# Kernel optimization log

Hardware: AMD Instinct MI355X
Metric: run time of the kernel (lower is better)

## Reference

```python
import jax, jax.numpy as jnp
import numpy as np

B, S, D, H = 4, 2048, 768, 8
HD = D // H
EPS = 1e-5
NEG = -1e9


def setup_inputs() -> dict:
    key = jax.random.key(0)
    ks = jax.random.split(key, 12)
    s = 1.0 / np.sqrt(D)
    inp = {
        "hidden_states": jax.random.normal(ks[0], (B, S, D), dtype=jnp.float32),
        "anchor_mask": jax.random.bernoulli(ks[1], 0.5, (B, S)),
        "ln_g": jnp.ones((D,), jnp.float32),
        "ln_b": jnp.zeros((D,), jnp.float32),
        "Wq": jax.random.uniform(ks[2], (D, D), jnp.float32, -s, s),
        "bq": jax.random.uniform(ks[3], (D,), jnp.float32, -s, s),
        "Wk": jax.random.uniform(ks[4], (D, D), jnp.float32, -s, s),
        "bk": jax.random.uniform(ks[5], (D,), jnp.float32, -s, s),
        "Wv": jax.random.uniform(ks[6], (D, D), jnp.float32, -s, s),
        "bv": jax.random.uniform(ks[7], (D,), jnp.float32, -s, s),
        "Wo": jax.random.uniform(ks[8], (D, D), jnp.float32, -s, s),
        "bo": jax.random.uniform(ks[9], (D,), jnp.float32, -s, s),
    }
    return inp


def reference(hidden_states, anchor_mask, ln_g, ln_b, Wq, bq, Wk, bk, Wv, bv, Wo, bo):
    # LayerNorm (per-token, so applying to all tokens == applying to gathered anchors)
    mu = jnp.mean(hidden_states, axis=-1, keepdims=True)
    var = jnp.mean(jnp.square(hidden_states - mu), axis=-1, keepdims=True)
    x = (hidden_states - mu) * jax.lax.rsqrt(var + EPS) * ln_g + ln_b

    # QKV projections: torch Linear is x @ W.T + b
    q = (jnp.einsum('bsd,ed->bse', x, Wq) + bq).reshape(B, S, H, HD)
    k = (jnp.einsum('bsd,ed->bse', x, Wk) + bk).reshape(B, S, H, HD)
    v = (jnp.einsum('bsd,ed->bse', x, Wv) + bv).reshape(B, S, H, HD)

    scale = 1.0 / np.sqrt(HD)
    scores = jnp.einsum('bqhd,bkhd->bhqk', q, k) * scale
    # keys restricted to anchor positions (equivalent to the gather)
    key_mask = anchor_mask[:, None, None, :]  # (B,1,1,S)
    scores = jnp.where(key_mask, scores, NEG)
    attn = jax.nn.softmax(scores, axis=-1)  # dropout is identity in eval

    out = jnp.einsum('bhqk,bkhd->bqhd', attn, v).reshape(B, S, D)
    out = jnp.einsum('bsd,ed->bse', out, Wo) + bo
    # scatter back: zeros at non-anchor positions
    return out * anchor_mask[:, :, None].astype(out.dtype)
```

## Files before the change

kernel.cpp:

```cpp
#include <hip/hip_runtime.h>
#include <math.h>

#define S_LEN 2048
#define D_DIM 768
#define NH 8
#define HD 96
#define NTOK 8192

typedef short bf16x8 __attribute__((ext_vector_type(8)));
typedef float f32x4 __attribute__((ext_vector_type(4)));
typedef float f32x16 __attribute__((ext_vector_type(16)));
typedef unsigned int u32x2 __attribute__((ext_vector_type(2)));
typedef unsigned int u32x4 __attribute__((ext_vector_type(4)));

__device__ __forceinline__ f32x4 mfma16(bf16x8 a, bf16x8 b, f32x4 c) {
    return __builtin_amdgcn_mfma_f32_16x16x32_bf16(a, b, c, 0, 0, 0);
}
__device__ __forceinline__ f32x16 mfma32(bf16x8 a, bf16x8 b, f32x16 c) {
    return __builtin_amdgcn_mfma_f32_32x32x16_bf16(a, b, c, 0, 0, 0);
}

__device__ __forceinline__ unsigned short f2bf(float f) {
    unsigned int u = __float_as_uint(f);
    u += 0x7fffu + ((u >> 16) & 1u);
    return (unsigned short)(u >> 16);
}

__device__ __forceinline__ unsigned int cvtpk(float lo, float hi) {
    unsigned int r;
    asm("v_cvt_pk_bf16_f32 %0, %1, %2" : "=v"(r) : "v"(lo), "v"(hi));
    return r;
}

__device__ __forceinline__ void gl_lds16(const unsigned short* g, unsigned short* l) {
    __builtin_amdgcn_global_load_lds(
        (const __attribute__((address_space(1))) unsigned int*)g,
        (__attribute__((address_space(3))) unsigned int*)l, 16, 0, 0);
}

#define TILE_SHORTS 6144
#define BH_SHORTS   196608

__global__ __launch_bounds__(256) void prep_kernel(
    const unsigned char* __restrict__ mb, int* __restrict__ idx, int* __restrict__ cnt,
    const float* __restrict__ Wq, const float* __restrict__ Wk,
    const float* __restrict__ Wv, const float* __restrict__ Wo,
    unsigned short* __restrict__ W4b, float* __restrict__ out)
{
    const int bi = blockIdx.x;
    const int t  = threadIdx.x;

    if (bi < 4) {
        __shared__ int red[4];
        __shared__ int warp_tot[4];
        const int b = bi;
        int s = 0;
        for (int i = t; i < NTOK; i += 256) s += (int)mb[i];
        for (int off = 32; off > 0; off >>= 1) s += __shfl_down(s, off, 64);
        if ((t & 63) == 0) red[t >> 6] = s;
        __syncthreads();
        const int total = red[0] + red[1] + red[2] + red[3];
        const int mode = (total > 20000) ? 2 : ((total > 2500) ? 1 : 0);
        const int*   mi = (const int*)mb;
        const float* mf = (const float*)mb;
        const int p0 = t * 8;
        int av = 0, c = 0;
        #pragma unroll
        for (int j = 0; j < 8; ++j) {
            const int g = b * S_LEN + p0 + j;
            bool a;
            if (mode == 2)      a = (mf[g] != 0.0f);
            else if (mode == 1) a = (mb[g] != 0);
            else                a = (mi[g] != 0);
            if (a) { av |= (1 << j); ++c; }
        }
        const int lane = t & 63, w = t >> 6;
        int v = c;
        #pragma unroll
        for (int off = 1; off < 64; off <<= 1) {
            const int u = __shfl_up(v, off, 64);
            if (lane >= off) v += u;
        }
        if (lane == 63) warp_tot[w] = v;
        __syncthreads();
        int wbase = 0;
        for (int i = 0; i < w; ++i) wbase += warp_tot[i];
        int o = wbase + v - c;
        #pragma unroll
        for (int j = 0; j < 8; ++j)
            if (av & (1 << j)) idx[b * S_LEN + (o++)] = p0 + j;
        if (t == 255) cnt[b] = wbase + v;
    } else if (bi < 1156) {
        const int i = bi - 4;
        const int w = i / 288, blk = i % 288;
        const float* src = (w == 0) ? Wq : (w == 1) ? Wk : (w == 2) ? Wv : Wo;
        const int base = (blk * 256 + t) * 8;
        const float4 a = *(const float4*)&src[base];
        const float4 c = *(const float4*)&src[base + 4];
        uint4 u;
        u.x = (unsigned int)f2bf(a.x) | ((unsigned int)f2bf(a.y) << 16);
        u.y = (unsigned int)f2bf(a.z) | ((unsigned int)f2bf(a.w) << 16);
        u.z = (unsigned int)f2bf(c.x) | ((unsigned int)f2bf(c.y) << 16);
        u.w = (unsigned int)f2bf(c.z) | ((unsigned int)f2bf(c.w) << 16);
        *(uint4*)&W4b[(size_t)w * 589824 + base] = u;
    } else {
        const size_t i4 = (size_t)(bi - 1156) * 256 + t;
        float4 z; z.x = z.y = z.z = z.w = 0.0f;
        *(float4*)&out[i4 * 4] = z;
    }
}

__global__ __launch_bounds__(256) void ln_gather_kernel(
    const float* __restrict__ H, const float* __restrict__ g,
    const float* __restrict__ bta, const int* __restrict__ idx,
    const int* __restrict__ cnt, unsigned short* __restrict__ X)
{
    __shared__ float rs[4], rss[4];
    const int slot = blockIdx.x;
    const int b = slot >> 11, r = slot & (S_LEN - 1);
    if (r >= cnt[b]) return;
    const int p = idx[slot];
    const float* hr = H + (size_t)(b * S_LEN + p) * D_DIM;
    unsigned short* xr = X + (size_t)slot * D_DIM;
    const int t = threadIdx.x;
    const float v0 = hr[t], v1 = hr[t + 256], v2 = hr[t + 512];
    float s  = v0 + v1 + v2;
    float ss = v0*v0 + v1*v1 + v2*v2;
    for (int off = 32; off > 0; off >>= 1) {
        s  += __shfl_down(s,  off, 64);
        ss += __shfl_down(ss, off, 64);
    }
    if ((t & 63) == 0) { rs[t >> 6] = s; rss[t >> 6] = ss; }
    __syncthreads();
    const float sum = rs[0] + rs[1] + rs[2] + rs[3];
    const float sq  = rss[0] + rss[1] + rss[2] + rss[3];
    const float mu  = sum * (1.0f / D_DIM);
    const float var = sq * (1.0f / D_DIM) - mu * mu;
    const float rstd = rsqrtf(var + 1e-5f);
    xr[t]       = f2bf((v0 - mu) * rstd * g[t]       + bta[t]);
    xr[t + 256] = f2bf((v1 - mu) * rstd * g[t + 256] + bta[t + 256]);
    xr[t + 512] = f2bf((v2 - mu) * rstd * g[t + 512] + bta[t + 512]);
}

__global__ __launch_bounds__(256) void gemm_bf16(
    const unsigned short* __restrict__ A,
    const unsigned short* __restrict__ W4,
    const float* __restrict__ b0, const float* __restrict__ b1,
    const float* __restrict__ b2,
    const int* __restrict__ cnt, const int* __restrict__ idx,
    unsigned short* __restrict__ Qo, unsigned short* __restrict__ Kp,
    unsigned short* __restrict__ Vp, float* __restrict__ Fo,
    int oproj)
{
    const int z = blockIdx.z;
    const int m0 = blockIdx.y * 64;
    const int b  = m0 >> 11;
    const int rbase = m0 & (S_LEN - 1);
    const int nc = cnt[b];
    if (rbase >= nc) return;
    const int n0 = blockIdx.x * 128;
    const unsigned short* W = W4 + (size_t)z * 589824;
    const float* bias = (z == 0) ? b0 : (z == 1 ? b1 : b2);

    __shared__ unsigned short Al[2][64 * 32];
    __shared__ unsigned short Bl[2][128 * 32];

    const int t = threadIdx.x;
    const int srow = t >> 2, sg = t & 3;
    const int ra0 = b * S_LEN + min(rbase + srow, nc - 1);
    const unsigned short* gA0 = A + (size_t)ra0 * 768 + sg * 8;
    const unsigned short* gB0 = W + (size_t)(n0 + srow)      * 768 + sg * 8;
    const unsigned short* gB1 = W + (size_t)(n0 + srow + 64) * 768 + sg * 8;
    const int t8 = t * 8;

    const int w = t >> 6, lane = t & 63;
    const int l15 = lane & 15, quad = lane >> 4;
    const int mh = (w & 1) * 32, nh2 = (w >> 1) * 64;

    f32x4 acc[2][4] = {};

    int aoff[2], boff[4];
    #pragma unroll
    for (int i = 0; i < 2; ++i) aoff[i] = (mh  + i * 16 + l15) * 32 + quad * 8;
    #pragma unroll
    for (int i = 0; i < 4; ++i) boff[i] = (nh2 + i * 16 + l15) * 32 + quad * 8;

    gl_lds16(gA0, &Al[0][t8]);
    gl_lds16(gB0, &Bl[0][t8]);
    gl_lds16(gB1, &Bl[0][2048 + t8]);
    __syncthreads();

    for (int it = 0; it < 24; ++it) {
        const int cur = it & 1;
        if (it + 1 < 24) {
            const int k1 = (it + 1) * 32;
            gl_lds16(gA0 + k1, &Al[cur ^ 1][t8]);
            gl_lds16(gB0 + k1, &Bl[cur ^ 1][t8]);
            gl_lds16(gB1 + k1, &Bl[cur ^ 1][2048 + t8]);
        }
        bf16x8 af[2], bfr[4];
        #pragma unroll
        for (int i = 0; i < 2; ++i) af[i]  = *(const bf16x8*)(&Al[cur][aoff[i]]);
        #pragma unroll
        for (int i = 0; i < 4; ++i) bfr[i] = *(const bf16x8*)(&Bl[cur][boff[i]]);
        #pragma unroll
        for (int ms = 0; ms < 2; ++ms)
            #pragma unroll
            for (int ns = 0; ns < 4; ++ns)
                acc[ms][ns] = mfma16(af[ms], bfr[ns], acc[ms][ns]);
        __syncthreads();
    }

    if (!oproj) {
        if (z == 0) {
            #pragma unroll
            for (int ns = 0; ns < 4; ++ns) {
                const int n = n0 + nh2 + ns * 16 + l15;
                const float bv = bias[n];
                #pragma unroll
                for (int ms = 0; ms < 2; ++ms) {
                    const int ml = mh + ms * 16 + quad * 4;
                    #pragma unroll
                    for (int r = 0; r < 4; ++r) {
                        const int slot = b * S_LEN + rbase + ml + r;
                        Qo[(size_t)slot * 768 + n] = f2bf(acc[ms][ns][r] + bv);
                    }
                }
            }
        } else if (z == 1) {
            #pragma unroll
            for (int ns = 0; ns < 4; ++ns) {
                const int n = n0 + nh2 + ns * 16 + l15;
                const int h = n / 96, d = n - h * 96;
                const float bv = bias[n];
                unsigned short* base = Kp + (size_t)(b * 8 + h) * BH_SHORTS;
                const int dseg = d >> 3, dlo = d & 7;
                #pragma unroll
                for (int ms = 0; ms < 2; ++ms) {
                    const int ml = mh + ms * 16 + quad * 4;
                    #pragma unroll
                    for (int r = 0; r < 4; ++r) {
                        const int tok = rbase + ml + r;
                        const int kt = tok >> 6, tk = tok & 63;
                        const int g16 = tk >> 4, lr = tk & 15;
                        base[(size_t)kt * TILE_SHORTS +
                             (g16 * 192 + dseg * 16 + lr) * 8 + dlo] =
                            (tok < nc) ? f2bf(acc[ms][ns][r] + bv)
                                       : (unsigned short)0;
                    }
                }
            }
        } else {
            #pragma unroll
            for (int ns = 0; ns < 4; ++ns) {
                const int n = n0 + nh2 + ns * 16 + l15;
                const int h = n / 96, d = n - h * 96;
                const float bv = bias[n];
                unsigned short* base = Vp + (size_t)(b * 8 + h) * BH_SHORTS;
                const int dg = d >> 4, l16 = d & 15;
                #pragma unroll
                for (int ms = 0; ms < 2; ++ms) {
                    const int ml = mh + ms * 16 + quad * 4;
                    const int k = rbase + ml;
                    const int kt = k >> 6, tk = k & 63;
                    const int kseg = tk >> 3, klo = tk & 7;
                    const unsigned short h0 =
                        (k + 0 < nc) ? f2bf(acc[ms][ns][0] + bv) : (unsigned short)0;
                    const unsigned short h1 =
                        (k + 1 < nc) ? f2bf(acc[ms][ns][1] + bv) : (unsigned short)0;
                    const unsigned short h2 =
                        (k + 2 < nc) ? f2bf(acc[ms][ns][2] + bv) : (unsigned short)0;
                    const unsigned short h3 =
                        (k + 3 < nc) ? f2bf(acc[ms][ns][3] + bv) : (unsigned short)0;
                    uint2 u;
                    u.x = (unsigned int)h0 | ((unsigned int)h1 << 16);
                    u.y = (unsigned int)h2 | ((unsigned int)h3 << 16);
                    *(uint2*)&base[(size_t)kt * TILE_SHORTS +
                                   (dg * 128 + kseg * 16 + l16) * 8 + klo] = u;
                }
            }
        }
    } else {
        #pragma unroll
        for (int ns = 0; ns < 4; ++ns) {
            const int n = n0 + nh2 + ns * 16 + l15;
            const float bv = bias[n];
            #pragma unroll
            for (int ms = 0; ms < 2; ++ms) {
                const int ml = mh + ms * 16 + quad * 4;
                #pragma unroll
                for (int r = 0; r < 4; ++r) {
                    const int rloc = rbase + ml + r;
                    if (rloc < nc) {
                        const int orow = b * S_LEN + idx[b * S_LEN + rloc];
                        Fo[(size_t)orow * 768 + n] = acc[ms][ns][r] + bv;
                    }
                }
            }
        }
    }
}

__global__ __launch_bounds__(256) void attn_mfma(
    const unsigned short* __restrict__ Q,
    const unsigned short* __restrict__ Kp,
    const unsigned short* __restrict__ Vp,
    const int* __restrict__ cnt,
    unsigned short* __restrict__ O)
{
    const int bh = blockIdx.x & 31;
    const int b  = bh >> 3, h = bh & 7;
    const int q0 = (blockIdx.x >> 5) * 32;
    const int nk = cnt[b];
    if (q0 >= nk) return;

    __shared__ f32x4 CMB4[2][64][13];

    const int t = threadIdx.x, w = t >> 6, lane = t & 63;
    const int l15 = lane & 15;
    const int gh  = (lane >> 4) & 1;
    const int hi  = lane >> 5;
    const int q32 = lane & 31;
    const int bS  = b * S_LEN;
    const float CE = 0.14724459f;

    const unsigned short* Kg = Kp + (size_t)(b * 8 + h) * BH_SHORTS;
    const unsigned short* Vg = Vp + (size_t)(b * 8 + h) * BH_SHORTS;

    const unsigned short* qrow = Q + (size_t)(bS + q0 + q32) * 768 + h * 96 + hi * 8;
    bf16x8 qf[6];
    #pragma unroll
    for (int ks = 0; ks < 6; ++ks) qf[ks] = *(const bf16x8*)(qrow + ks * 16);

    const int kb0 = (gh * 192 + hi * 16 + l15) * 8;
    const int vb0 = (gh * 128 + hi * 16 + l15) * 8;

    float ls0 = 0.0f, ls1 = 0.0f;
    f32x16 oacc[3] = {};

    const int kts = (nk + 63) >> 6;

    if (w < kts) {
        const unsigned short* Kt0 = Kg + (size_t)w * TILE_SHORTS + kb0;
        bf16x8 kfc[6];
        #pragma unroll
        for (int ks = 0; ks < 6; ++ks)
            kfc[ks] = *(const bf16x8*)(Kt0 + (ks * 32) * 8);

        for (int kt = w; kt < kts; kt += 4) {
            const unsigned short* Kt = Kg + (size_t)kt * TILE_SHORTS + kb0;
            const unsigned short* Vt = Vg + (size_t)kt * TILE_SHORTS + vb0;

            #pragma unroll
            for (int s = 0; s < 2; ++s) {
                const unsigned short* Kn = (s == 0)
                    ? (Kt + 384 * 8)
                    : (Kt + (size_t)4 * TILE_SHORTS);
                bf16x8 kfn[6];
                #pragma unroll
                for (int ks = 0; ks < 6; ++ks)
                    kfn[ks] = *(const bf16x8*)(Kn + (ks * 32) * 8);

                f32x16 sa = {};
                __builtin_amdgcn_s_setprio(1);
                #pragma unroll
                for (int ks = 0; ks < 6; ++ks) sa = mfma32(kfc[ks], qf[ks], sa);
                __builtin_amdgcn_s_setprio(0);

                unsigned int wv[8];
                #pragma unroll
                for (int j = 0; j < 8; ++j) {
                    const float e0 = exp2f(sa[2 * j]     * CE);
                    const float e1 = exp2f(sa[2 * j + 1] * CE);
                    if (j & 1) ls1 += e0 + e1; else ls0 += e0 + e1;
                    wv[j] = cvtpk(e0, e1);
                }
                const u32x2 r02 = __builtin_amdgcn_permlane32_swap(wv[0], wv[2], false, false);
                const u32x2 r13 = __builtin_amdgcn_permlane32_swap(wv[1], wv[3], false, false);
                const u32x2 r46 = __builtin_amdgcn_permlane32_swap(wv[4], wv[6], false, false);
                const u32x2 r57 = __builtin_amdgcn_permlane32_swap(wv[5], wv[7], false, false);
                const u32x4 pw0 = { r02.x, r13.x, r02.y, r13.y };
                const u32x4 pw1 = { r46.x, r57.x, r46.y, r57.y };
                const bf16x8 pb0 = __builtin_bit_cast(bf16x8, pw0);
                const bf16x8 pb1 = __builtin_bit_cast(bf16x8, pw1);

                const int kkb = s * 2;
                __builtin_amdgcn_s_setprio(1);
                #pragma unroll
                for (int dg = 0; dg < 3; ++dg) {
                    const bf16x8 v0 = *(const bf16x8*)(Vt + (dg * 256 + kkb * 32) * 8);
                    const bf16x8 v1 = *(const bf16x8*)(Vt + (dg * 256 + (kkb + 1) * 32) * 8);
                    oacc[dg] = mfma32(v0, pb0, oacc[dg]);
                    oacc[dg] = mfma32(v1, pb1, oacc[dg]);
                }
                __builtin_amdgcn_s_setprio(0);

                #pragma unroll
                for (int ks = 0; ks < 6; ++ks) kfc[ks] = kfn[ks];
            }
        }
    }

    float lsum = ls0 + ls1;
    lsum += __shfl_xor(lsum, 32);

    if (w >= 2) {
        f32x4* dst = CMB4[w - 2][lane];
        #pragma unroll
        for (int dg = 0; dg < 3; ++dg)
            #pragma unroll
            for (int m = 0; m < 4; ++m) {
                const f32x4 p = { oacc[dg][4 * m],     oacc[dg][4 * m + 1],
                                  oacc[dg][4 * m + 2], oacc[dg][4 * m + 3] };
                dst[dg * 4 + m] = p;
            }
        const f32x4 tl = { lsum, 0.0f, 0.0f, 0.0f };
        dst[12] = tl;
    }
    __syncthreads();
    if (w < 2) {
        const f32x4* src = CMB4[w][lane];
        #pragma unroll
        for (int dg = 0; dg < 3; ++dg)
            #pragma unroll
            for (int m = 0; m < 4; ++m) {
                const f32x4 p = src[dg * 4 + m];
                #pragma unroll
                for (int j = 0; j < 4; ++j) oacc[dg][4 * m + j] += p[j];
            }
        lsum += src[12][0];
    }
    __syncthreads();
    if (w == 1) {
        f32x4* dst = CMB4[0][lane];
        #pragma unroll
        for (int dg = 0; dg < 3; ++dg)
            #pragma unroll
            for (int m = 0; m < 4; ++m) {
                const f32x4 p = { oacc[dg][4 * m],     oacc[dg][4 * m + 1],
                                  oacc[dg][4 * m + 2], oacc[dg][4 * m + 3] };
                dst[dg * 4 + m] = p;
            }
        const f32x4 tl = { lsum, 0.0f, 0.0f, 0.0f };
        dst[12] = tl;
    }
    __syncthreads();
    if (w > 0) return;

    {
        const f32x4* src = CMB4[0][lane];
        #pragma unroll
        for (int dg = 0; dg < 3; ++dg)
            #pragma unroll
            for (int m = 0; m < 4; ++m) {
                const f32x4 p = src[dg * 4 + m];
                #pragma unroll
                for (int j = 0; j < 4; ++j) oacc[dg][4 * m + j] += p[j];
            }
        lsum += src[12][0];
    }
    lsum -= (float)((kts << 6) - nk);

    const int qi = q0 + q32;
    if (qi < nk) {
        const float rl = 1.0f / lsum;
        unsigned short* og = O + (size_t)(bS + qi) * 768 + h * 96;
        #pragma unroll
        for (int dg = 0; dg < 3; ++dg) {
            #pragma unroll
            for (int m = 0; m < 4; ++m) {
                uint2 u;
                u.x = cvtpk(oacc[dg][4 * m]     * rl, oacc[dg][4 * m + 1] * rl);
                u.y = cvtpk(oacc[dg][4 * m + 2] * rl, oacc[dg][4 * m + 3] * rl);
                *(uint2*)&og[dg * 32 + m * 8 + hi * 4] = u;
            }
        }
    }
}

extern "C" void kernel_launch(void* const* d_in, const int* in_sizes, int n_in,
                              void* d_out, int out_size, void* d_ws, size_t ws_size,
                              hipStream_t stream)
{
    const float* hs  = (const float*)d_in[0];
    const unsigned char* am = (const unsigned char*)d_in[1];
    const float* lng = (const float*)d_in[2];
    const float* lnb = (const float*)d_in[3];
    const float* Wq  = (const float*)d_in[4];
    const float* bq  = (const float*)d_in[5];
    const float* Wk  = (const float*)d_in[6];
    const float* bk  = (const float*)d_in[7];
    const float* Wv  = (const float*)d_in[8];
    const float* bv  = (const float*)d_in[9];
    const float* Wo  = (const float*)d_in[10];
    const float* bo  = (const float*)d_in[11];

    char* ws = (char*)d_ws;
    const size_t BUF = (size_t)NTOK * 768 * 2;
    int* idx = (int*)ws;
    int* cnt = (int*)(ws + 32768);
    unsigned short* xb  = (unsigned short*)(ws + 65536);
    unsigned short* Qb  = (unsigned short*)(ws + 65536 + BUF);
    unsigned short* Kpb = (unsigned short*)(ws + 65536 + 2 * BUF);
    unsigned short* Vpb = (unsigned short*)(ws + 65536 + 3 * BUF);
    unsigned short* W4b = (unsigned short*)(ws + 65536 + 4 * BUF);
    unsigned short* Ob  = xb;
    float* out = (float*)d_out;

    prep_kernel<<<dim3(2692), dim3(256), 0, stream>>>(
        am, idx, cnt, Wq, Wk, Wv, Wo, W4b, out);

    ln_gather_kernel<<<dim3(NTOK), dim3(256), 0, stream>>>(hs, lng, lnb, idx, cnt, xb);

    gemm_bf16<<<dim3(6, 128, 3), dim3(256), 0, stream>>>(
        xb, W4b, bq, bk, bv, cnt, idx, Qb, Kpb, Vpb, nullptr, 0);

    attn_mfma<<<dim3(2048), dim3(256), 0, stream>>>(Qb, Kpb, Vpb, cnt, Ob);

    gemm_bf16<<<dim3(6, 128, 1), dim3(256), 0, stream>>>(
        Ob, W4b + (size_t)3 * 589824, bo, bo, bo, cnt, idx,
        nullptr, nullptr, nullptr, out, 1);
}
```

Measured before the change: 200.5 us.

## Use explicit vmcnt waits in GEMM loop and drop K register prefetch in attention

```diff
diff --git a/kernel.cpp b/kernel.cpp
--- a/kernel.cpp
+++ b/kernel.cpp
@@ -188,7 +188,9 @@
     gl_lds16(gA0, &Al[0][t8]);
     gl_lds16(gB0, &Bl[0][t8]);
     gl_lds16(gB1, &Bl[0][2048 + t8]);
-    __syncthreads();
+    asm volatile("s_waitcnt vmcnt(0)" ::: "memory");
+    __builtin_amdgcn_s_barrier();
+    __builtin_amdgcn_sched_barrier(0);
 
     for (int it = 0; it < 24; ++it) {
         const int cur = it & 1;
@@ -197,7 +199,13 @@
             gl_lds16(gA0 + k1, &Al[cur ^ 1][t8]);
             gl_lds16(gB0 + k1, &Bl[cur ^ 1][t8]);
             gl_lds16(gB1 + k1, &Bl[cur ^ 1][2048 + t8]);
-        }
+            asm volatile("s_waitcnt vmcnt(3)" ::: "memory");
+        } else {
+            asm volatile("s_waitcnt vmcnt(0)" ::: "memory");
+        }
+        __builtin_amdgcn_s_barrier();
+        __builtin_amdgcn_sched_barrier(0);
+
         bf16x8 af[2], bfr[4];
         #pragma unroll
         for (int i = 0; i < 2; ++i) af[i]  = *(const bf16x8*)(&Al[cur][aoff[i]]);
@@ -208,7 +216,9 @@
             #pragma unroll
             for (int ns = 0; ns < 4; ++ns)
                 acc[ms][ns] = mfma16(af[ms], bfr[ns], acc[ms][ns]);
-        __syncthreads();
+
+        __builtin_amdgcn_sched_barrier(0);
+        __builtin_amdgcn_s_barrier();
     }
 
     if (!oproj) {
@@ -340,64 +350,49 @@
 
     const int kts = (nk + 63) >> 6;
 
-    if (w < kts) {
-        const unsigned short* Kt0 = Kg + (size_t)w * TILE_SHORTS + kb0;
-        bf16x8 kfc[6];
-        #pragma unroll
-        for (int ks = 0; ks < 6; ++ks)
-            kfc[ks] = *(const bf16x8*)(Kt0 + (ks * 32) * 8);
-
-        for (int kt = w; kt < kts; kt += 4) {
-            const unsigned short* Kt = Kg + (size_t)kt * TILE_SHORTS + kb0;
-            const unsigned short* Vt = Vg + (size_t)kt * TILE_SHORTS + vb0;
-
-            #pragma unroll
-            for (int s = 0; s < 2; ++s) {
-                const unsigned short* Kn = (s == 0)
-                    ? (Kt + 384 * 8)
-                    : (Kt + (size_t)4 * TILE_SHORTS);
-                bf16x8 kfn[6];
-                #pragma unroll
-                for (int ks = 0; ks < 6; ++ks)
-                    kfn[ks] = *(const bf16x8*)(Kn + (ks * 32) * 8);
-
-                f32x16 sa = {};
-                __builtin_amdgcn_s_setprio(1);
-                #pragma unroll
-                for (int ks = 0; ks < 6; ++ks) sa = mfma32(kfc[ks], qf[ks], sa);
-                __builtin_amdgcn_s_setprio(0);
-
-                unsigned int wv[8];
-                #pragma unroll
-                for (int j = 0; j < 8; ++j) {
-                    const float e0 = exp2f(sa[2 * j]     * CE);
-                    const float e1 = exp2f(sa[2 * j + 1] * CE);
-                    if (j & 1) ls1 += e0 + e1; else ls0 += e0 + e1;
-                    wv[j] = cvtpk(e0, e1);
-                }
-                const u32x2 r02 = __builtin_amdgcn_permlane32_swap(wv[0], wv[2], false, false);
-                const u32x2 r13 = __builtin_amdgcn_permlane32_swap(wv[1], wv[3], false, false);
-                const u32x2 r46 = __builtin_amdgcn_permlane32_swap(wv[4], wv[6], false, false);
-                const u32x2 r57 = __builtin_amdgcn_permlane32_swap(wv[5], wv[7], false, false);
-                const u32x4 pw0 = { r02.x, r13.x, r02.y, r13.y };
-                const u32x4 pw1 = { r46.x, r57.x, r46.y, r57.y };
-                const bf16x8 pb0 = __builtin_bit_cast(bf16x8, pw0);
-                const bf16x8 pb1 = __builtin_bit_cast(bf16x8, pw1);
-
-                const int kkb = s * 2;
-                __builtin_amdgcn_s_setprio(1);
-                #pragma unroll
-                for (int dg = 0; dg < 3; ++dg) {
-                    const bf16x8 v0 = *(const bf16x8*)(Vt + (dg * 256 + kkb * 32) * 8);
-                    const bf16x8 v1 = *(const bf16x8*)(Vt + (dg * 256 + (kkb + 1) * 32) * 8);
-                    oacc[dg] = mfma32(v0, pb0, oacc[dg]);
-                    oacc[dg] = mfma32(v1, pb1, oacc[dg]);
-                }
-                __builtin_amdgcn_s_setprio(0);
-
-                #pragma unroll
-                for (int ks = 0; ks < 6; ++ks) kfc[ks] = kfn[ks];
-            }
+    for (int kt = w; kt < kts; kt += 4) {
+        const unsigned short* Kt = Kg + (size_t)kt * TILE_SHORTS + kb0;
+        const unsigned short* Vt = Vg + (size_t)kt * TILE_SHORTS + vb0;
+
+        #pragma unroll
+        for (int s = 0; s < 2; ++s) {
+            bf16x8 kf[6];
+            #pragma unroll
+            for (int ks = 0; ks < 6; ++ks)
+                kf[ks] = *(const bf16x8*)(Kt + (s * 384 + ks * 32) * 8);
+            f32x16 sa = {};
+            __builtin_amdgcn_s_setprio(1);
+            #pragma unroll
+            for (int ks = 0; ks < 6; ++ks) sa = mfma32(kf[ks], qf[ks], sa);
+            __builtin_amdgcn_s_setprio(0);
+
+            unsigned int wv[8];
+            #pragma unroll
+            for (int j = 0; j < 8; ++j) {
+                const float e0 = exp2f(sa[2 * j]     * CE);
+                const float e1 = exp2f(sa[2 * j + 1] * CE);
+                if (j & 1) ls1 += e0 + e1; else ls0 += e0 + e1;
+                wv[j] = cvtpk(e0, e1);
+            }
+            const u32x2 r02 = __builtin_amdgcn_permlane32_swap(wv[0], wv[2], false, false);
+            const u32x2 r13 = __builtin_amdgcn_permlane32_swap(wv[1], wv[3], false, false);
+            const u32x2 r46 = __builtin_amdgcn_permlane32_swap(wv[4], wv[6], false, false);
+            const u32x2 r57 = __builtin_amdgcn_permlane32_swap(wv[5], wv[7], false, false);
+            const u32x4 pw0 = { r02.x, r13.x, r02.y, r13.y };
+            const u32x4 pw1 = { r46.x, r57.x, r46.y, r57.y };
+            const bf16x8 pb0 = __builtin_bit_cast(bf16x8, pw0);
+            const bf16x8 pb1 = __builtin_bit_cast(bf16x8, pw1);
+
+            const int kkb = s * 2;
+            __builtin_amdgcn_s_setprio(1);
+            #pragma unroll
+            for (int dg = 0; dg < 3; ++dg) {
+                const bf16x8 v0 = *(const bf16x8*)(Vt + (dg * 256 + kkb * 32) * 8);
+                const bf16x8 v1 = *(const bf16x8*)(Vt + (dg * 256 + (kkb + 1) * 32) * 8);
+                oacc[dg] = mfma32(v0, pb0, oacc[dg]);
+                oacc[dg] = mfma32(v1, pb1, oacc[dg]);
+            }
+            __builtin_amdgcn_s_setprio(0);
         }
     }
 
```

Measured after the change: 192.4 us. -4.0%, faster.
